# Kernel optimization log

Measured on AMD Instinct MI355X. Metric: run time of the kernel, lower is better.

The kernel has to match this reference:

```python
import jax, jax.numpy as jnp
import numpy as np

B, C, N = 2, 256, 4096
EPS = 1e-5
TEMPERATURE = float(C) ** 0.5  # inchannel ** 0.5 from __init__


def conv1x1(x, w, b=None):
    # x: (B,C_in,N,1), w: (C_out,C_in)
    y = jnp.einsum('oi,binj->bonj', w, x)
    if b is not None:
        y = y + b[None, :, None, None]
    return y


def instance_norm(x):
    # InstanceNorm2d, affine=False: per-sample, per-channel over spatial dims
    m = x.mean(axis=(2, 3), keepdims=True)
    v = x.var(axis=(2, 3), keepdims=True)
    return (x - m) * jax.lax.rsqrt(v + EPS)


def batch_norm(x, w, b):
    # BatchNorm2d in training mode: stats over (batch, spatial)
    m = x.mean(axis=(0, 2, 3), keepdims=True)
    v = x.var(axis=(0, 2, 3), keepdims=True)
    return (x - m) * jax.lax.rsqrt(v + EPS) * w[None, :, None, None] + b[None, :, None, None]


def setup_inputs() -> dict:
    key = jax.random.key(0)
    ks = jax.random.split(key, 8)
    s = 1.0 / np.sqrt(C)
    inp = {
        'x': jax.random.normal(ks[0], (B, C, N, 1), dtype=jnp.float32),
        'edge_map': jax.random.randint(ks[1], (B, N, N), 0, 2, dtype=jnp.int32),
        'edge_attr': jax.random.uniform(ks[2], (B, N, N), dtype=jnp.float32),
        # self.linear: Conv2d(C,C,1,bias=False)
        'linear_w': jax.random.normal(ks[3], (C, C), dtype=jnp.float32) * s,
        # ffn.right: Conv2d(C,C,1) + BatchNorm2d
        'w_r': jax.random.normal(ks[4], (C, C), dtype=jnp.float32) * s,
        'b_r': jnp.zeros((C,), jnp.float32),
        'bn_r_w': jnp.ones((C,), jnp.float32),
        'bn_r_b': jnp.zeros((C,), jnp.float32),
        # ffn.left: Conv2d -> IN -> BN -> ReLU -> Conv2d -> IN -> BN
        'w1': jax.random.normal(ks[5], (C, C), dtype=jnp.float32) * s,
        'b1': jnp.zeros((C,), jnp.float32),
        'bn1_w': jnp.ones((C,), jnp.float32),
        'bn1_b': jnp.zeros((C,), jnp.float32),
        'w2': jax.random.normal(ks[6], (C, C), dtype=jnp.float32) * s,
        'b2': jnp.zeros((C,), jnp.float32),
        'bn2_w': jnp.ones((C,), jnp.float32),
        'bn2_b': jnp.zeros((C,), jnp.float32),
    }
    return inp


def reference(x, edge_map, edge_attr, linear_w, w_r, b_r, bn_r_w, bn_r_b,
              w1, b1, bn1_w, bn1_b, w2, b2, bn2_w, bn2_b):
    # feat = self.linear(x); q = k = feat; v = elu(feat)
    feat = conv1x1(x, linear_w)            # (B,C,N,1)
    q = feat[..., 0]                       # (B,C,N)
    v = jax.nn.elu(q)                      # (B,C,N)

    # attention logits, scaled by edge_attr, masked softmax over adjacency
    logits = jnp.einsum('bdn,bdm->bnm', q, q) / TEMPERATURE
    logits = edge_attr * logits
    mask = edge_map.astype(bool)
    logits = jnp.where(mask, logits, -jnp.inf)
    attn = jax.nn.softmax(logits, axis=-1)
    attn = jnp.where(mask, attn, 0.0)

    # val = attn @ v^T -> (B,N,C), unsqueeze(1), InstanceNorm2d
    val = jnp.matmul(attn, jnp.swapaxes(v, 1, 2))[:, None]  # (B,1,N,C)
    val = instance_norm(val)

    # feat_attn = attn.transpose(1,3) + x  -> (B,C,N,1)
    feat_attn = jnp.swapaxes(val, 1, 3) + x

    # ResNet_Block (pre=True)
    x1 = batch_norm(conv1x1(feat_attn, w_r, b_r), bn_r_w, bn_r_b)
    out = conv1x1(feat_attn, w1, b1)
    out = batch_norm(instance_norm(out), bn1_w, bn1_b)
    out = jax.nn.relu(out)
    out = conv1x1(out, w2, b2)
    out = batch_norm(instance_norm(out), bn2_w, bn2_b)
    return jax.nn.relu(out + x1)
```

## Files before the change

kernel.cpp:

```cpp
#include <hip/hip_runtime.h>
#include <hip/hip_bf16.h>
#include <cstdint>
#include <cstddef>

constexpr int B_N = 2;
constexpr int C_N = 256;
constexpr int N_N = 4096;
constexpr int NC  = N_N * C_N;
constexpr float EPS_  = 1e-5f;
constexpr float INV_T = 1.0f / 16.0f;

using bf16x8 = __attribute__((ext_vector_type(8))) __bf16;
using f32x4  = __attribute__((ext_vector_type(4))) float;
using i32x4  = __attribute__((ext_vector_type(4))) int;

typedef __attribute__((address_space(1))) const void g1_void;
typedef __attribute__((address_space(3))) void l3_void;

__device__ __forceinline__ uint16_t f2bf(float f) {
  uint32_t u = __builtin_bit_cast(uint32_t, f);
  u += 0x7fffu + ((u >> 16) & 1u);
  return (uint16_t)(u >> 16);
}
__device__ __forceinline__ float bf2f(uint16_t h) {
  return __builtin_bit_cast(float, (uint32_t)h << 16);
}

__global__ __launch_bounds__(256) void cast_w_kernel(
    const float* __restrict__ w0, const float* __restrict__ w1,
    const float* __restrict__ w2, const float* __restrict__ w3,
    uint16_t* __restrict__ o0, uint16_t* __restrict__ o1,
    uint16_t* __restrict__ o2, uint16_t* __restrict__ o3) {
  int i = blockIdx.x * 256 + threadIdx.x;
  int m = blockIdx.y;
  const float* s = (m == 0) ? w0 : (m == 1) ? w1 : (m == 2) ? w2 : w3;
  uint16_t* d = (m == 0) ? o0 : (m == 1) ? o1 : (m == 2) ? o2 : o3;
  d[i] = f2bf(s[i]);
}

__global__ __launch_bounds__(256) void transpose_x_kernel(
    const float* __restrict__ x, uint16_t* __restrict__ xtb) {
  __shared__ float tile[32][33];
  int b = blockIdx.z;
  int c0 = blockIdx.x * 32, n0 = blockIdx.y * 32;
  int tc = threadIdx.x & 31, tr = threadIdx.x >> 5;
  const float* xb = x + (size_t)b * C_N * N_N;
#pragma unroll
  for (int pp = 0; pp < 4; pp++) {
    int r = tr + pp * 8;
    tile[r][tc] = xb[(size_t)(c0 + r) * N_N + n0 + tc];
  }
  __syncthreads();
  uint16_t* xtbp = xtb + (size_t)b * NC;
#pragma unroll
  for (int pp = 0; pp < 4; pp++) {
    int r = tr + pp * 8;
    xtbp[(size_t)(n0 + r) * C_N + c0 + tc] = f2bf(tile[tc][r]);
  }
}

__global__ __launch_bounds__(256) void gemm_kernel(
    const uint16_t* __restrict__ Wb, const uint16_t* __restrict__ Xb,
    const float* __restrict__ bias, float* __restrict__ Yt) {
  int b = blockIdx.z;
  int n0 = blockIdx.x * 64;
  int c0 = blockIdx.y * 64;
  int w = threadIdx.x >> 6;
  int l = threadIdx.x & 63;
  int lr = l & 15, g = l >> 4;
  const uint16_t* xp = Xb + (size_t)b * NC;
  f32x4 acc[4] = {{0.f,0.f,0.f,0.f},{0.f,0.f,0.f,0.f},{0.f,0.f,0.f,0.f},{0.f,0.f,0.f,0.f}};
  const uint16_t* wrow = Wb + (size_t)(c0 + w * 16 + lr) * C_N + g * 8;
#pragma unroll
  for (int kk = 0; kk < 8; kk++) {
    bf16x8 a = *(const bf16x8*)(wrow + kk * 32);
#pragma unroll
    for (int j = 0; j < 4; j++) {
      bf16x8 bb = *(const bf16x8*)(xp + (size_t)(n0 + j * 16 + lr) * C_N + kk * 32 + g * 8);
      acc[j] = __builtin_amdgcn_mfma_f32_16x16x32_bf16(a, bb, acc[j], 0, 0, 0);
    }
  }
  int cw = c0 + w * 16 + g * 4;
  f32x4 bs = {0.f, 0.f, 0.f, 0.f};
  if (bias) { bs[0] = bias[cw]; bs[1] = bias[cw + 1]; bs[2] = bias[cw + 2]; bs[3] = bias[cw + 3]; }
  float* yp = Yt + (size_t)b * NC;
#pragma unroll
  for (int j = 0; j < 4; j++) {
    int n = n0 + j * 16 + lr;
    f32x4 v = acc[j] + bs;
    *(f32x4*)(yp + (size_t)n * C_N + cw) = v;
  }
}

__global__ __launch_bounds__(256) void gemm_dual_kernel(
    const uint16_t* __restrict__ Wb1, const uint16_t* __restrict__ Wb2,
    const uint16_t* __restrict__ Xb,
    const float* __restrict__ bias1, const float* __restrict__ bias2,
    float* __restrict__ Y1, float* __restrict__ Y2) {
  int b = blockIdx.z;
  int n0 = blockIdx.x * 64;
  int c0 = blockIdx.y * 64;
  int w = threadIdx.x >> 6;
  int l = threadIdx.x & 63;
  int lr = l & 15, g = l >> 4;
  const uint16_t* xp = Xb + (size_t)b * NC;
  f32x4 acc1[4] = {{0.f,0.f,0.f,0.f},{0.f,0.f,0.f,0.f},{0.f,0.f,0.f,0.f},{0.f,0.f,0.f,0.f}};
  f32x4 acc2[4] = {{0.f,0.f,0.f,0.f},{0.f,0.f,0.f,0.f},{0.f,0.f,0.f,0.f},{0.f,0.f,0.f,0.f}};
  const uint16_t* wrow1 = Wb1 + (size_t)(c0 + w * 16 + lr) * C_N + g * 8;
  const uint16_t* wrow2 = Wb2 + (size_t)(c0 + w * 16 + lr) * C_N + g * 8;
#pragma unroll
  for (int kk = 0; kk < 8; kk++) {
    bf16x8 a1 = *(const bf16x8*)(wrow1 + kk * 32);
    bf16x8 a2 = *(const bf16x8*)(wrow2 + kk * 32);
#pragma unroll
    for (int j = 0; j < 4; j++) {
      bf16x8 bb = *(const bf16x8*)(xp + (size_t)(n0 + j * 16 + lr) * C_N + kk * 32 + g * 8);
      acc1[j] = __builtin_amdgcn_mfma_f32_16x16x32_bf16(a1, bb, acc1[j], 0, 0, 0);
      acc2[j] = __builtin_amdgcn_mfma_f32_16x16x32_bf16(a2, bb, acc2[j], 0, 0, 0);
    }
  }
  int cw = c0 + w * 16 + g * 4;
  f32x4 bs1 = { bias1[cw], bias1[cw + 1], bias1[cw + 2], bias1[cw + 3] };
  f32x4 bs2 = { bias2[cw], bias2[cw + 1], bias2[cw + 2], bias2[cw + 3] };
  float* y1p = Y1 + (size_t)b * NC;
  float* y2p = Y2 + (size_t)b * NC;
#pragma unroll
  for (int j = 0; j < 4; j++) {
    int n = n0 + j * 16 + lr;
    f32x4 v1 = acc1[j] + bs1;
    f32x4 v2 = acc2[j] + bs2;
    *(f32x4*)(y1p + (size_t)n * C_N + cw) = v1;
    *(f32x4*)(y2p + (size_t)n * C_N + cw) = v2;
  }
}

__global__ __launch_bounds__(256) void qv_kernel(
    const float* __restrict__ feat, uint16_t* __restrict__ qt, uint16_t* __restrict__ vcn) {
  __shared__ float tile[32][33];
  int b = blockIdx.z;
  int n0 = blockIdx.x * 32, c0 = blockIdx.y * 32;
  int tc = threadIdx.x & 31, tr = threadIdx.x >> 5;
  const float* fb = feat + (size_t)b * NC;
  uint16_t* qb = qt + (size_t)b * NC;
#pragma unroll
  for (int pp = 0; pp < 4; pp++) {
    int r = tr + pp * 8;
    float v = fb[(size_t)(n0 + r) * C_N + c0 + tc];
    qb[(size_t)(n0 + r) * C_N + c0 + tc] = f2bf(v);
    tile[r][tc] = v;
  }
  __syncthreads();
  uint16_t* vbp = vcn + (size_t)b * NC;
#pragma unroll
  for (int pp = 0; pp < 4; pp++) {
    int r = tr + pp * 8;
    float v = tile[tc][r];
    float e = v > 0.f ? v : (__expf(v) - 1.f);
    vbp[(size_t)(c0 + r) * N_N + n0 + tc] = f2bf(e);
  }
}

__global__ __launch_bounds__(256, 4) void qk_kernel(
    const uint16_t* __restrict__ qt, const float* __restrict__ ea,
    const int* __restrict__ em, uint16_t* __restrict__ P,
    float* __restrict__ rowsum, int mlen) {
  __shared__ uint16_t alds[2][32 * 256];
  int b = blockIdx.z;
  int mstart = blockIdx.y * mlen;
  int nb = blockIdx.x * 64;
  int w = threadIdx.x >> 6, l = threadIdx.x & 63;
  int lr = l & 15, g = l >> 4;
  int n = nb + w * 16 + lr;
  const uint16_t* qb = qt + (size_t)b * NC;
  uint16_t* Pb = P + (size_t)b * N_N * N_N;
  const size_t ebase = (size_t)b * N_N * N_N + (size_t)n * N_N;

  bf16x8 qa[8];
#pragma unroll
  for (int kk = 0; kk < 8; kk++)
    qa[kk] = *(const bf16x8*)(qb + (size_t)n * C_N + kk * 32 + g * 8);

  auto STAGE = [&](int t) {
    int m0 = mstart + t * 32;
    uint16_t* buf = alds[t & 1];
#pragma unroll
    for (int q = 0; q < 4; q++) {
      int chunk = w * 4 + q;
      int row_local = chunk * 2 + (l >> 5);
      int cb = l & 31;
      int src_cb = cb ^ (row_local & 7);
      const uint16_t* src = qb + (size_t)(m0 + row_local) * C_N + src_cb * 8;
      __builtin_amdgcn_global_load_lds((g1_void*)src, (l3_void*)(buf + chunk * 512), 16, 0, 0);
    }
  };
  auto EDGES = [&](int t, i32x4* em4, f32x4* ea4) {
    int m0 = mstart + t * 32;
    const size_t erow = ebase + m0 + g * 4;
#pragma unroll
    for (int j = 0; j < 2; j++) {
      em4[j] = __builtin_nontemporal_load((const i32x4*)(em + erow + j * 16));
      ea4[j] = __builtin_nontemporal_load((const f32x4*)(ea + erow + j * 16));
    }
  };

  i32x4 emc[2], emn[2]; f32x4 eac[2], ean[2];
  STAGE(0);
  EDGES(0, emc, eac);

  float rs = 0.f;
  const int NT = mlen / 32;
  int sw = lr & 7;
  for (int t = 0; t < NT; ++t) {
    if (t == 0) { asm volatile("s_waitcnt vmcnt(4)" ::: "memory"); }
    else        { asm volatile("s_waitcnt vmcnt(6)" ::: "memory"); }
    __builtin_amdgcn_s_barrier();
    __builtin_amdgcn_sched_barrier(0);
    if (t + 1 < NT) { STAGE(t + 1); EDGES(t + 1, emn, ean); }
    const uint16_t* buf = alds[t & 1];
    f32x4 acc[2] = {{0.f,0.f,0.f,0.f},{0.f,0.f,0.f,0.f}};
#pragma unroll
    for (int kk = 0; kk < 8; kk++) {
#pragma unroll
      for (int j = 0; j < 2; j++) {
        int cb = (kk * 4 + g) ^ sw;
        bf16x8 qm = *(const bf16x8*)(buf + (j * 16 + lr) * 256 + cb * 8);
        acc[j] = __builtin_amdgcn_mfma_f32_16x16x32_bf16(qm, qa[kk], acc[j], 0, 0, 0);
      }
    }
    int m0 = mstart + t * 32;
#pragma unroll
    for (int j = 0; j < 2; j++) {
      uint16_t pk[4];
#pragma unroll
      for (int r = 0; r < 4; r++) {
        float p = emc[j][r] ? __expf(eac[j][r] * acc[j][r] * INV_T) : 0.f;
        rs += p;
        pk[r] = f2bf(p);
      }
      uint2 st;
      st.x = (uint32_t)pk[0] | ((uint32_t)pk[1] << 16);
      st.y = (uint32_t)pk[2] | ((uint32_t)pk[3] << 16);
      *(uint2*)(Pb + (size_t)n * N_N + m0 + j * 16 + g * 4) = st;
    }
    emc[0] = emn[0]; emc[1] = emn[1];
    eac[0] = ean[0]; eac[1] = ean[1];
    __builtin_amdgcn_sched_barrier(0);
  }
  rs += __shfl_xor(rs, 16, 64);
  rs += __shfl_xor(rs, 32, 64);
  if (l < 16)
    atomicAdd(&rowsum[(size_t)b * N_N + n], rs);
}

__global__ __launch_bounds__(256, 4) void pv_kernel(
    const uint16_t* __restrict__ P, const uint16_t* __restrict__ vcn,
    float* __restrict__ Opart, int klen) {
  __shared__ uint16_t plds[2][64 * 32];
  __shared__ uint16_t vlds[2][256 * 32];
  int b = blockIdx.z;
  int n0 = blockIdx.x * 64;
  int mbase = blockIdx.y * klen;
  int w = threadIdx.x >> 6, l = threadIdx.x & 63;
  int lr = l & 15, g = l >> 4;
  const uint16_t* Pb = P + (size_t)b * N_N * N_N;
  const uint16_t* vb = vcn + (size_t)b * NC;

  auto STAGE = [&](int t) {
    int m0 = mbase + t * 32;
    uint16_t* pbuf = plds[t & 1];
    uint16_t* vbuf = vlds[t & 1];
    {
      int row = w * 16 + (l >> 2);
      int seg = (l & 3) ^ (row & 3);
      const uint16_t* src = Pb + (size_t)(n0 + row) * N_N + m0 + seg * 8;
      __builtin_amdgcn_global_load_lds((g1_void*)src, (l3_void*)(pbuf + w * 512), 16, 0, 0);
    }
#pragma unroll
    for (int q = 0; q < 4; q++) {
      int c = (w * 4 + q) * 16 + (l >> 2);
      int seg = (l & 3) ^ (c & 3);
      const uint16_t* src = vb + (size_t)c * N_N + m0 + seg * 8;
      __builtin_amdgcn_global_load_lds((g1_void*)src, (l3_void*)(vbuf + (w * 4 + q) * 512), 16, 0, 0);
    }
  };

  f32x4 acc[4][4];
#pragma unroll
  for (int t = 0; t < 4; t++)
#pragma unroll
    for (int j = 0; j < 4; j++) acc[t][j] = (f32x4){0.f, 0.f, 0.f, 0.f};

  STAGE(0);
  const int NT = klen / 32;
  int sw = lr & 3;
  for (int t = 0; t < NT; ++t) {
    if (t + 1 < NT) STAGE(t + 1);
    if (t + 1 < NT) { asm volatile("s_waitcnt vmcnt(5)" ::: "memory"); }
    else            { asm volatile("s_waitcnt vmcnt(0)" ::: "memory"); }
    __builtin_amdgcn_s_barrier();
    __builtin_amdgcn_sched_barrier(0);
    const uint16_t* pbuf = plds[t & 1];
    const uint16_t* vbuf = vlds[t & 1];
    bf16x8 bv[4], av[4];
#pragma unroll
    for (int j = 0; j < 4; j++)
      bv[j] = *(const bf16x8*)(pbuf + (j * 16 + lr) * 32 + (g ^ sw) * 8);
#pragma unroll
    for (int tt = 0; tt < 4; tt++)
      av[tt] = *(const bf16x8*)(vbuf + (w * 64 + tt * 16 + lr) * 32 + (g ^ sw) * 8);
#pragma unroll
    for (int tt = 0; tt < 4; tt++)
#pragma unroll
      for (int j = 0; j < 4; j++)
        acc[tt][j] = __builtin_amdgcn_mfma_f32_16x16x32_bf16(av[tt], bv[j], acc[tt][j], 0, 0, 0);
    __builtin_amdgcn_s_barrier();
    __builtin_amdgcn_sched_barrier(0);
  }
  float* op = Opart + ((size_t)blockIdx.y * B_N + b) * NC;
#pragma unroll
  for (int tt = 0; tt < 4; tt++) {
    int cw = w * 64 + tt * 16 + g * 4;
#pragma unroll
    for (int j = 0; j < 4; j++) {
      int n = n0 + j * 16 + lr;
      *(f32x4*)(op + (size_t)n * C_N + cw) = acc[tt][j];
    }
  }
}

__global__ __launch_bounds__(256) void combine_kernel(
    const float* __restrict__ Op, const float* __restrict__ rowsum,
    float* __restrict__ val, float* __restrict__ vstats, int split) {
  size_t idx = ((size_t)blockIdx.x * 256 + threadIdx.x) * 4;
  int b = (int)(idx / NC);
  size_t inb = idx - (size_t)b * NC;
  size_t n = inb / C_N;
  f32x4 acc = {0.f, 0.f, 0.f, 0.f};
  for (int s = 0; s < split; s++)
    acc += *(const f32x4*)(Op + (size_t)(s * B_N + b) * NC + inb);
  float lt = rowsum[(size_t)b * N_N + n];
  float invl = lt > 0.f ? 1.f / lt : 0.f;
  acc *= invl;
  *(f32x4*)(val + idx) = acc;
  float s1 = acc[0] + acc[1] + acc[2] + acc[3];
  float s2 = acc[0]*acc[0] + acc[1]*acc[1] + acc[2]*acc[2] + acc[3]*acc[3];
  for (int off = 32; off; off >>= 1) { s1 += __shfl_down(s1, off, 64); s2 += __shfl_down(s2, off, 64); }
  __shared__ float r1[4], r2[4];
  int w = threadIdx.x >> 6;
  if ((threadIdx.x & 63) == 0) { r1[w] = s1; r2[w] = s2; }
  __syncthreads();
  if (threadIdx.x == 0) {
    atomicAdd(&vstats[b * 2],     r1[0] + r1[1] + r1[2] + r1[3]);
    atomicAdd(&vstats[b * 2 + 1], r2[0] + r2[1] + r2[2] + r2[3]);
  }
}

__global__ __launch_bounds__(256) void fa_kernel(
    const float* __restrict__ val, const float* __restrict__ vstats,
    uint16_t* __restrict__ fab) {
  size_t idx = ((size_t)blockIdx.x * 256 + threadIdx.x) * 4;
  int b = (int)(idx / NC);
  float mean = vstats[b * 2] * (1.f / NC);
  float var = vstats[b * 2 + 1] * (1.f / NC) - mean * mean;
  float inv = rsqrtf(var + EPS_);
  f32x4 v = *(const f32x4*)(val + idx);
  uint2 xr = *(const uint2*)(fab + idx);
  float xv[4] = { bf2f((uint16_t)(xr.x & 0xffff)), bf2f((uint16_t)(xr.x >> 16)),
                  bf2f((uint16_t)(xr.y & 0xffff)), bf2f((uint16_t)(xr.y >> 16)) };
  uint16_t ov[4];
#pragma unroll
  for (int j = 0; j < 4; j++) ov[j] = f2bf((v[j] - mean) * inv + xv[j]);
  uint2 pk;
  pk.x = (uint32_t)ov[0] | ((uint32_t)ov[1] << 16);
  pk.y = (uint32_t)ov[2] | ((uint32_t)ov[3] << 16);
  *(uint2*)(fab + idx) = pk;
}

__global__ __launch_bounds__(256) void colstats_dual_kernel(
    const float* __restrict__ Ya, float* __restrict__ outa,
    const float* __restrict__ Yb, float* __restrict__ outb) {
  const float* Y = blockIdx.y ? Yb : Ya;
  float* out = blockIdx.y ? outb : outa;
  int perBatch = blockIdx.y;
  int c = threadIdx.x;
  size_t r0 = (size_t)blockIdx.x * 64;
  float s1 = 0.f, s2 = 0.f;
  const float* base = Y + r0 * C_N + c;
  for (int r = 0; r < 64; r++) { float v = base[(size_t)r * C_N]; s1 += v; s2 += v * v; }
  int b = perBatch ? (int)(r0 / N_N) : 0;
  atomicAdd(&out[(b * C_N + c) * 2], s1);
  atomicAdd(&out[(b * C_N + c) * 2 + 1], s2);
}

__global__ __launch_bounds__(256) void colstats_kernel(
    const float* __restrict__ Y, float* __restrict__ out, int perBatch) {
  int c = threadIdx.x;
  size_t r0 = (size_t)blockIdx.x * 64;
  float s1 = 0.f, s2 = 0.f;
  const float* base = Y + r0 * C_N + c;
  for (int r = 0; r < 64; r++) { float v = base[(size_t)r * C_N]; s1 += v; s2 += v * v; }
  int b = perBatch ? (int)(r0 / N_N) : 0;
  atomicAdd(&out[(b * C_N + c) * 2], s1);
  atomicAdd(&out[(b * C_N + c) * 2 + 1], s2);
}

__global__ __launch_bounds__(256) void h_kernel(
    const float* __restrict__ y1, const float* __restrict__ st,
    const float* __restrict__ bw, const float* __restrict__ bb, uint16_t* __restrict__ h) {
  size_t idx = ((size_t)blockIdx.x * 256 + threadIdx.x) * 4;
  int b = (int)(idx / NC);
  int c = (int)(idx % C_N);
  f32x4 y = *(const f32x4*)(y1 + idx);
  uint16_t ov[4];
#pragma unroll
  for (int j = 0; j < 4; j++) {
    int cc = c + j;
    float m0 = st[(0 * C_N + cc) * 2] * (1.f / N_N);
    float v0 = st[(0 * C_N + cc) * 2 + 1] * (1.f / N_N) - m0 * m0;
    float m1 = st[(1 * C_N + cc) * 2] * (1.f / N_N);
    float v1 = st[(1 * C_N + cc) * 2 + 1] * (1.f / N_N) - m1 * m1;
    float mb = b ? m1 : m0, vb = b ? v1 : v0;
    float vc = 0.5f * (v0 / (v0 + EPS_) + v1 / (v1 + EPS_));
    float val = (y[j] - mb) * rsqrtf(vb + EPS_) * rsqrtf(vc + EPS_) * bw[cc] + bb[cc];
    ov[j] = f2bf(fmaxf(val, 0.f));
  }
  uint2 pk;
  pk.x = (uint32_t)ov[0] | ((uint32_t)ov[1] << 16);
  pk.y = (uint32_t)ov[2] | ((uint32_t)ov[3] << 16);
  *(uint2*)(h + idx) = pk;
}

__global__ __launch_bounds__(256) void final_kernel(
    const float* __restrict__ y2, const float* __restrict__ yr,
    const float* __restrict__ st2, const float* __restrict__ strr,
    const float* __restrict__ g2, const float* __restrict__ be2,
    const float* __restrict__ gr, const float* __restrict__ ber, float* __restrict__ out) {
  __shared__ float t[32][33];
  int b = blockIdx.z;
  int n0 = blockIdx.x * 32, c0 = blockIdx.y * 32;
  int tc = threadIdx.x & 31, tr = threadIdx.x >> 5;
  int c = c0 + tc;
  float m20 = st2[(0 * C_N + c) * 2] * (1.f / N_N);
  float v20 = st2[(0 * C_N + c) * 2 + 1] * (1.f / N_N) - m20 * m20;
  float m21 = st2[(1 * C_N + c) * 2] * (1.f / N_N);
  float v21 = st2[(1 * C_N + c) * 2 + 1] * (1.f / N_N) - m21 * m21;
  float mb = b ? m21 : m20, vb = b ? v21 : v20;
  float inb = rsqrtf(vb + EPS_);
  float vc2 = 0.5f * (v20 / (v20 + EPS_) + v21 / (v21 + EPS_));
  float sc2 = rsqrtf(vc2 + EPS_) * g2[c];
  float mr = strr[c * 2] * (1.f / (B_N * N_N));
  float vr = strr[c * 2 + 1] * (1.f / (B_N * N_N)) - mr * mr;
  float scr = rsqrtf(vr + EPS_) * gr[c];
  const float* y2b = y2 + (size_t)b * NC;
  const float* yrb = yr + (size_t)b * NC;
#pragma unroll
  for (int pp = 0; pp < 4; pp++) {
    int r = tr + pp * 8;
    size_t off = (size_t)(n0 + r) * C_N + c;
    float a = (y2b[off] - mb) * inb * sc2 + be2[c];
    float x1 = (yrb[off] - mr) * scr + ber[c];
    t[r][tc] = fmaxf(a + x1, 0.f);
  }
  __syncthreads();
  float* ob = out + (size_t)b * C_N * N_N;
#pragma unroll
  for (int pp = 0; pp < 4; pp++) {
    int r = tr + pp * 8;
    ob[(size_t)(c0 + r) * N_N + n0 + tc] = t[tc][r];
  }
}

extern "C" void kernel_launch(void* const* d_in, const int* in_sizes, int n_in,
                              void* d_out, int out_size, void* d_ws, size_t ws_size,
                              hipStream_t stream) {
  (void)in_sizes; (void)n_in; (void)out_size;
  const float* x    = (const float*)d_in[0];
  const int*   em   = (const int*)  d_in[1];
  const float* ea   = (const float*)d_in[2];
  const float* lw   = (const float*)d_in[3];
  const float* wr   = (const float*)d_in[4];
  const float* br   = (const float*)d_in[5];
  const float* bnrw = (const float*)d_in[6];
  const float* bnrb = (const float*)d_in[7];
  const float* w1   = (const float*)d_in[8];
  const float* b1   = (const float*)d_in[9];
  const float* bn1w = (const float*)d_in[10];
  const float* bn1b = (const float*)d_in[11];
  const float* w2   = (const float*)d_in[12];
  const float* b2   = (const float*)d_in[13];
  const float* bn2w = (const float*)d_in[14];
  const float* bn2b = (const float*)d_in[15];

  char* p = (char*)d_ws;
  auto alloc = [&](size_t bytes) -> char* {
    char* r = p; p += (bytes + 255) & ~(size_t)255; return r;
  };
  uint16_t* xtb = (uint16_t*)alloc(2ULL * B_N * NC);
  uint16_t* qt  = (uint16_t*)alloc(2ULL * B_N * NC);
  uint16_t* vcn = (uint16_t*)alloc(2ULL * B_N * NC);
  uint16_t* wb0 = (uint16_t*)alloc(2ULL * C_N * C_N);
  uint16_t* wb1 = (uint16_t*)alloc(2ULL * C_N * C_N);
  uint16_t* wb2 = (uint16_t*)alloc(2ULL * C_N * C_N);
  uint16_t* wb3 = (uint16_t*)alloc(2ULL * C_N * C_N);
  constexpr int STATS_F = 4 + 512 + 1024 + 1024;
  constexpr int RS_F = B_N * N_N;
  float* stats = (float*)alloc(sizeof(float) * (STATS_F + RS_F));
  float* vstats = stats;
  float* strr   = stats + 4;
  float* st1    = strr + 512;
  float* st2    = st1 + 1024;
  float* rowsum = stats + STATS_F;
  uint16_t* P = (uint16_t*)alloc(2ULL * B_N * (size_t)N_N * N_N);
  float* feat = (float*)P;
  float* yr   = (float*)((char*)P + (8ULL << 20));
  float* y2   = (float*)((char*)P + (16ULL << 20));
  float* y1   = (float*)((char*)P + (24ULL << 20));
  size_t fixed = (size_t)(p - (char*)d_ws);
  size_t partsz = sizeof(float) * (size_t)B_N * NC;
  int SPLITK = 4;
  while (SPLITK > 1 && fixed + (size_t)SPLITK * partsz > ws_size) SPLITK >>= 1;
  float* Opart = (float*)alloc((size_t)SPLITK * partsz);

  (void)hipMemsetAsync(stats, 0, sizeof(float) * (STATS_F + RS_F), stream);

  cast_w_kernel<<<dim3(C_N * C_N / 256, 4, 1), 256, 0, stream>>>(lw, wr, w1, w2, wb0, wb1, wb2, wb3);
  transpose_x_kernel<<<dim3(C_N / 32, N_N / 32, B_N), 256, 0, stream>>>(x, xtb);
  gemm_kernel<<<dim3(N_N / 64, C_N / 64, B_N), 256, 0, stream>>>(wb0, xtb, nullptr, feat);
  qv_kernel<<<dim3(N_N / 32, C_N / 32, B_N), 256, 0, stream>>>(feat, qt, vcn);
  qk_kernel<<<dim3(N_N / 64, 8, B_N), 256, 0, stream>>>(qt, ea, em, P, rowsum, N_N / 8);
  pv_kernel<<<dim3(N_N / 64, SPLITK, B_N), 256, 0, stream>>>(P, vcn, Opart, N_N / SPLITK);
  combine_kernel<<<dim3((size_t)B_N * NC / 1024), 256, 0, stream>>>(Opart, rowsum, feat, vstats, SPLITK);
  fa_kernel<<<dim3((size_t)B_N * NC / 1024), 256, 0, stream>>>(feat, vstats, xtb);
  gemm_dual_kernel<<<dim3(N_N / 64, C_N / 64, B_N), 256, 0, stream>>>(wb1, wb2, xtb, br, b1, yr, y1);
  colstats_dual_kernel<<<dim3(B_N * N_N / 64, 2), 256, 0, stream>>>(yr, strr, y1, st1);
  h_kernel<<<dim3((size_t)B_N * NC / 1024), 256, 0, stream>>>(y1, st1, bn1w, bn1b, qt);
  gemm_kernel<<<dim3(N_N / 64, C_N / 64, B_N), 256, 0, stream>>>(wb3, qt, b2, y2);
  colstats_kernel<<<dim3(B_N * N_N / 64), 256, 0, stream>>>(y2, st2, 1);
  final_kernel<<<dim3(N_N / 32, C_N / 32, B_N), 256, 0, stream>>>(
      y2, yr, st2, strr, bn2w, bn2b, bnrw, bnrb, (float*)d_out);
}
```

Before: 272.3 us.

## Fuse QK-softmax and PV into a single flash-style attention kernel

```diff
diff --git a/kernel.cpp b/kernel.cpp
--- a/kernel.cpp
+++ b/kernel.cpp
@@ -160,11 +160,13 @@
   }
 }
 
-__global__ __launch_bounds__(256, 4) void qk_kernel(
-    const uint16_t* __restrict__ qt, const float* __restrict__ ea,
-    const int* __restrict__ em, uint16_t* __restrict__ P,
-    float* __restrict__ rowsum, int mlen) {
+__global__ __launch_bounds__(256, 2) void attn_fused_kernel(
+    const uint16_t* __restrict__ qt, const uint16_t* __restrict__ vcn,
+    const float* __restrict__ ea, const int* __restrict__ em,
+    float* __restrict__ Opart, float* __restrict__ rowsum, int mlen) {
   __shared__ uint16_t alds[2][32 * 256];
+  __shared__ uint16_t vlds[2][256 * 32];
+  __shared__ uint16_t plds[64 * 32];
   int b = blockIdx.z;
   int mstart = blockIdx.y * mlen;
   int nb = blockIdx.x * 64;
@@ -172,7 +174,7 @@
   int lr = l & 15, g = l >> 4;
   int n = nb + w * 16 + lr;
   const uint16_t* qb = qt + (size_t)b * NC;
-  uint16_t* Pb = P + (size_t)b * N_N * N_N;
+  const uint16_t* vb = vcn + (size_t)b * NC;
   const size_t ebase = (size_t)b * N_N * N_N + (size_t)n * N_N;
 
   bf16x8 qa[8];
@@ -182,7 +184,7 @@
 
   auto STAGE = [&](int t) {
     int m0 = mstart + t * 32;
-    uint16_t* buf = alds[t & 1];
+    uint16_t* abuf = alds[t & 1];
 #pragma unroll
     for (int q = 0; q < 4; q++) {
       int chunk = w * 4 + q;
@@ -190,7 +192,15 @@
       int cb = l & 31;
       int src_cb = cb ^ (row_local & 7);
       const uint16_t* src = qb + (size_t)(m0 + row_local) * C_N + src_cb * 8;
-      __builtin_amdgcn_global_load_lds((g1_void*)src, (l3_void*)(buf + chunk * 512), 16, 0, 0);
+      __builtin_amdgcn_global_load_lds((g1_void*)src, (l3_void*)(abuf + chunk * 512), 16, 0, 0);
+    }
+    uint16_t* vbuf = vlds[t & 1];
+#pragma unroll
+    for (int q = 0; q < 4; q++) {
+      int c = (w * 4 + q) * 16 + (l >> 2);
+      int seg = (l & 3) ^ (c & 3);
+      const uint16_t* src = vb + (size_t)c * N_N + m0 + seg * 8;
+      __builtin_amdgcn_global_load_lds((g1_void*)src, (l3_void*)(vbuf + (w * 4 + q) * 512), 16, 0, 0);
     }
   };
   auto EDGES = [&](int t, i32x4* em4, f32x4* ea4) {
@@ -207,27 +217,31 @@
   STAGE(0);
   EDGES(0, emc, eac);
 
+  f32x4 accp[4][4];
+#pragma unroll
+  for (int tt = 0; tt < 4; tt++)
+#pragma unroll
+    for (int j = 0; j < 4; j++) accp[tt][j] = (f32x4){0.f, 0.f, 0.f, 0.f};
   float rs = 0.f;
   const int NT = mlen / 32;
-  int sw = lr & 7;
+  int swA = lr & 7;
+  int swP = lr & 3;
   for (int t = 0; t < NT; ++t) {
-    if (t == 0) { asm volatile("s_waitcnt vmcnt(4)" ::: "memory"); }
-    else        { asm volatile("s_waitcnt vmcnt(6)" ::: "memory"); }
+    asm volatile("s_waitcnt vmcnt(4)" ::: "memory");
     __builtin_amdgcn_s_barrier();
     __builtin_amdgcn_sched_barrier(0);
     if (t + 1 < NT) { STAGE(t + 1); EDGES(t + 1, emn, ean); }
-    const uint16_t* buf = alds[t & 1];
+    const uint16_t* abuf = alds[t & 1];
     f32x4 acc[2] = {{0.f,0.f,0.f,0.f},{0.f,0.f,0.f,0.f}};
 #pragma unroll
     for (int kk = 0; kk < 8; kk++) {
 #pragma unroll
       for (int j = 0; j < 2; j++) {
-        int cb = (kk * 4 + g) ^ sw;
-        bf16x8 qm = *(const bf16x8*)(buf + (j * 16 + lr) * 256 + cb * 8);
+        int cb = (kk * 4 + g) ^ swA;
+        bf16x8 qm = *(const bf16x8*)(abuf + (j * 16 + lr) * 256 + cb * 8);
         acc[j] = __builtin_amdgcn_mfma_f32_16x16x32_bf16(qm, qa[kk], acc[j], 0, 0, 0);
       }
     }
-    int m0 = mstart + t * 32;
 #pragma unroll
     for (int j = 0; j < 2; j++) {
       uint16_t pk[4];
@@ -240,92 +254,41 @@
       uint2 st;
       st.x = (uint32_t)pk[0] | ((uint32_t)pk[1] << 16);
       st.y = (uint32_t)pk[2] | ((uint32_t)pk[3] << 16);
-      *(uint2*)(Pb + (size_t)n * N_N + m0 + j * 16 + g * 4) = st;
+      *(uint2*)(plds + (w * 16 + lr) * 32 + (((2 * j + (g >> 1)) ^ swP) * 8) + (g & 1) * 4) = st;
     }
     emc[0] = emn[0]; emc[1] = emn[1];
     eac[0] = ean[0]; eac[1] = ean[1];
+    __builtin_amdgcn_s_barrier();
     __builtin_amdgcn_sched_barrier(0);
+    const uint16_t* vbuf = vlds[t & 1];
+    bf16x8 bv[4], av[4];
+#pragma unroll
+    for (int j = 0; j < 4; j++)
+      bv[j] = *(const bf16x8*)(plds + (j * 16 + lr) * 32 + ((g ^ swP) * 8));
+#pragma unroll
+    for (int tt = 0; tt < 4; tt++)
+      av[tt] = *(const bf16x8*)(vbuf + (w * 64 + tt * 16 + lr) * 32 + ((g ^ swP) * 8));
+#pragma unroll
+    for (int tt = 0; tt < 4; tt++)
+#pragma unroll
+      for (int j = 0; j < 4; j++)
+        accp[tt][j] = __builtin_amdgcn_mfma_f32_16x16x32_bf16(av[tt], bv[j], accp[tt][j], 0, 0, 0);
+    __builtin_amdgcn_sched_barrier(0);
+  }
+  float* op = Opart + ((size_t)blockIdx.y * B_N + b) * NC;
+#pragma unroll
+  for (int tt = 0; tt < 4; tt++) {
+    int cw = w * 64 + tt * 16 + g * 4;
+#pragma unroll
+    for (int j = 0; j < 4; j++) {
+      int nn = nb + j * 16 + lr;
+      *(f32x4*)(op + (size_t)nn * C_N + cw) = accp[tt][j];
+    }
   }
   rs += __shfl_xor(rs, 16, 64);
   rs += __shfl_xor(rs, 32, 64);
   if (l < 16)
     atomicAdd(&rowsum[(size_t)b * N_N + n], rs);
-}
-
-__global__ __launch_bounds__(256, 4) void pv_kernel(
-    const uint16_t* __restrict__ P, const uint16_t* __restrict__ vcn,
-    float* __restrict__ Opart, int klen) {
-  __shared__ uint16_t plds[2][64 * 32];
-  __shared__ uint16_t vlds[2][256 * 32];
-  int b = blockIdx.z;
-  int n0 = blockIdx.x * 64;
-  int mbase = blockIdx.y * klen;
-  int w = threadIdx.x >> 6, l = threadIdx.x & 63;
-  int lr = l & 15, g = l >> 4;
-  const uint16_t* Pb = P + (size_t)b * N_N * N_N;
-  const uint16_t* vb = vcn + (size_t)b * NC;
-
-  auto STAGE = [&](int t) {
-    int m0 = mbase + t * 32;
-    uint16_t* pbuf = plds[t & 1];
-    uint16_t* vbuf = vlds[t & 1];
-    {
-      int row = w * 16 + (l >> 2);
-      int seg = (l & 3) ^ (row & 3);
-      const uint16_t* src = Pb + (size_t)(n0 + row) * N_N + m0 + seg * 8;
-      __builtin_amdgcn_global_load_lds((g1_void*)src, (l3_void*)(pbuf + w * 512), 16, 0, 0);
-    }
-#pragma unroll
-    for (int q = 0; q < 4; q++) {
-      int c = (w * 4 + q) * 16 + (l >> 2);
-      int seg = (l & 3) ^ (c & 3);
-      const uint16_t* src = vb + (size_t)c * N_N + m0 + seg * 8;
-      __builtin_amdgcn_global_load_lds((g1_void*)src, (l3_void*)(vbuf + (w * 4 + q) * 512), 16, 0, 0);
-    }
-  };
-
-  f32x4 acc[4][4];
-#pragma unroll
-  for (int t = 0; t < 4; t++)
-#pragma unroll
-    for (int j = 0; j < 4; j++) acc[t][j] = (f32x4){0.f, 0.f, 0.f, 0.f};
-
-  STAGE(0);
-  const int NT = klen / 32;
-  int sw = lr & 3;
-  for (int t = 0; t < NT; ++t) {
-    if (t + 1 < NT) STAGE(t + 1);
-    if (t + 1 < NT) { asm volatile("s_waitcnt vmcnt(5)" ::: "memory"); }
-    else            { asm volatile("s_waitcnt vmcnt(0)" ::: "memory"); }
-    __builtin_amdgcn_s_barrier();
-    __builtin_amdgcn_sched_barrier(0);
-    const uint16_t* pbuf = plds[t & 1];
-    const uint16_t* vbuf = vlds[t & 1];
-    bf16x8 bv[4], av[4];
-#pragma unroll
-    for (int j = 0; j < 4; j++)
-      bv[j] = *(const bf16x8*)(pbuf + (j * 16 + lr) * 32 + (g ^ sw) * 8);
-#pragma unroll
-    for (int tt = 0; tt < 4; tt++)
-      av[tt] = *(const bf16x8*)(vbuf + (w * 64 + tt * 16 + lr) * 32 + (g ^ sw) * 8);
-#pragma unroll
-    for (int tt = 0; tt < 4; tt++)
-#pragma unroll
-      for (int j = 0; j < 4; j++)
-        acc[tt][j] = __builtin_amdgcn_mfma_f32_16x16x32_bf16(av[tt], bv[j], acc[tt][j], 0, 0, 0);
-    __builtin_amdgcn_s_barrier();
-    __builtin_amdgcn_sched_barrier(0);
-  }
-  float* op = Opart + ((size_t)blockIdx.y * B_N + b) * NC;
-#pragma unroll
-  for (int tt = 0; tt < 4; tt++) {
-    int cw = w * 64 + tt * 16 + g * 4;
-#pragma unroll
-    for (int j = 0; j < 4; j++) {
-      int n = n0 + j * 16 + lr;
-      *(f32x4*)(op + (size_t)n * C_N + cw) = acc[tt][j];
-    }
-  }
 }
 
 __global__ __launch_bounds__(256) void combine_kernel(
@@ -510,11 +473,10 @@
   float* st1    = strr + 512;
   float* st2    = st1 + 1024;
   float* rowsum = stats + STATS_F;
-  uint16_t* P = (uint16_t*)alloc(2ULL * B_N * (size_t)N_N * N_N);
-  float* feat = (float*)P;
-  float* yr   = (float*)((char*)P + (8ULL << 20));
-  float* y2   = (float*)((char*)P + (16ULL << 20));
-  float* y1   = (float*)((char*)P + (24ULL << 20));
+  float* feat = (float*)alloc(sizeof(float) * (size_t)B_N * NC);
+  float* yr   = (float*)alloc(sizeof(float) * (size_t)B_N * NC);
+  float* y2   = (float*)alloc(sizeof(float) * (size_t)B_N * NC);
+  float* y1   = (float*)alloc(sizeof(float) * (size_t)B_N * NC);
   size_t fixed = (size_t)(p - (char*)d_ws);
   size_t partsz = sizeof(float) * (size_t)B_N * NC;
   int SPLITK = 4;
@@ -527,8 +489,8 @@
   transpose_x_kernel<<<dim3(C_N / 32, N_N / 32, B_N), 256, 0, stream>>>(x, xtb);
   gemm_kernel<<<dim3(N_N / 64, C_N / 64, B_N), 256, 0, stream>>>(wb0, xtb, nullptr, feat);
   qv_kernel<<<dim3(N_N / 32, C_N / 32, B_N), 256, 0, stream>>>(feat, qt, vcn);
-  qk_kernel<<<dim3(N_N / 64, 8, B_N), 256, 0, stream>>>(qt, ea, em, P, rowsum, N_N / 8);
-  pv_kernel<<<dim3(N_N / 64, SPLITK, B_N), 256, 0, stream>>>(P, vcn, Opart, N_N / SPLITK);
+  attn_fused_kernel<<<dim3(N_N / 64, SPLITK, B_N), 256, 0, stream>>>(
+      qt, vcn, ea, em, Opart, rowsum, N_N / SPLITK);
   combine_kernel<<<dim3((size_t)B_N * NC / 1024), 256, 0, stream>>>(Opart, rowsum, feat, vstats, SPLITK);
   fa_kernel<<<dim3((size_t)B_N * NC / 1024), 256, 0, stream>>>(feat, vstats, xtb);
   gemm_dual_kernel<<<dim3(N_N / 64, C_N / 64, B_N), 256, 0, stream>>>(wb1, wb2, xtb, br, b1, yr, y1);
```

Result: faster. 242.5 us (median of 3 runs) (-11.0%).
